# Optimization experiments

Hardware: AMD Instinct MI355X
Metric: run time of the kernel (lower is better)

## Reference

```python
import jax, jax.numpy as jnp
import numpy as np

OBS_DIM = 4096
NUM_ACTIONS = 18
ACTION_DIM = 64
D_MODEL = 512
N_LAYERS = 4
HIST = 256
BATCH = 32
D_STATE = 16
D_CONV = 4
EXPAND = 2
D_INNER = EXPAND * D_MODEL           # 1024
DT_RANK = -(-D_MODEL // 16)          # ceil(512/16)=32
OBS_OUT = D_MODEL - ACTION_DIM       # 448


def setup_inputs() -> dict:
    key = jax.random.key(0)
    ks = jax.random.split(key, 16)
    s = 0.02
    inp = {
        "obss": jax.random.normal(ks[0], (BATCH, HIST, OBS_DIM), jnp.float32),
        "actions": jax.random.randint(ks[1], (BATCH, HIST, 1), 0, NUM_ACTIONS),
        "obs_W": jax.random.normal(ks[2], (OBS_OUT, OBS_DIM), jnp.float32) * s,
        "obs_b": jnp.zeros((OBS_OUT,), jnp.float32),
        "act_emb": jax.random.normal(ks[3], (NUM_ACTIONS, ACTION_DIM), jnp.float32) * s,
        "pos_emb": jax.random.normal(ks[4], (1, HIST, D_MODEL), jnp.float32) * s,
        # stacked Mamba params, leading dim = N_LAYERS
        "W_in": jax.random.normal(ks[5], (N_LAYERS, 2 * D_INNER, D_MODEL), jnp.float32) * s,
        "conv_w": jax.random.normal(ks[6], (N_LAYERS, D_INNER, D_CONV), jnp.float32) * s,
        "conv_b": jnp.zeros((N_LAYERS, D_INNER), jnp.float32),
        "W_x": jax.random.normal(ks[7], (N_LAYERS, DT_RANK + 2 * D_STATE, D_INNER), jnp.float32) * s,
        "W_dt": jax.random.normal(ks[8], (N_LAYERS, D_INNER, DT_RANK), jnp.float32) * s,
        "b_dt": jnp.full((N_LAYERS, D_INNER), -4.6, jnp.float32),  # softplus(-4.6)~0.01
        "A_log": jnp.log(jnp.broadcast_to(jnp.arange(1, D_STATE + 1, dtype=jnp.float32), (N_LAYERS, D_INNER, D_STATE))),
        "D_p": jnp.ones((N_LAYERS, D_INNER), jnp.float32),
        "W_out": jax.random.normal(ks[9], (N_LAYERS, D_MODEL, D_INNER), jnp.float32) * s,
        "ffn_W1": jax.random.normal(ks[10], (D_MODEL, D_MODEL), jnp.float32) * s,
        "ffn_b1": jnp.zeros((D_MODEL,), jnp.float32),
        "ffn_W2": jax.random.normal(ks[11], (NUM_ACTIONS, D_MODEL), jnp.float32) * s,
        "ffn_b2": jnp.zeros((NUM_ACTIONS,), jnp.float32),
    }
    return inp


def mamba_block(x, W_in, conv_w, conv_b, W_x, W_dt, b_dt, A_log, D_p, W_out):
    # x: (B, L, D_MODEL)
    B_, L, _ = x.shape
    xz = jnp.einsum('bld,ed->ble', x, W_in)            # (B,L,2*Di)
    xi, z = jnp.split(xz, 2, axis=-1)
    # causal depthwise conv1d, kernel D_CONV
    xp = jnp.pad(xi, ((0, 0), (D_CONV - 1, 0), (0, 0)))
    xc = conv_b + sum(conv_w[:, k] * xp[:, k:k + L, :] for k in range(D_CONV))
    xc = jax.nn.silu(xc)                               # (B,L,Di)
    xdbl = jnp.einsum('bld,ed->ble', xc, W_x)          # (B,L,dt_rank+2*ds)
    dt, Bm, Cm = jnp.split(xdbl, [DT_RANK, DT_RANK + D_STATE], axis=-1)
    dt = jax.nn.softplus(jnp.einsum('blr,dr->bld', dt, W_dt) + b_dt)  # (B,L,Di)
    A = -jnp.exp(A_log)                                # (Di,ds)

    def step(h, inp):
        dt_t, B_t, C_t, x_t = inp                      # (B,Di),(B,ds),(B,ds),(B,Di)
        dA = jnp.exp(dt_t[:, :, None] * A)             # (B,Di,ds)
        h = dA * h + dt_t[:, :, None] * B_t[:, None, :] * x_t[:, :, None]
        y = jnp.einsum('bdn,bn->bd', h, C_t)
        return h, y

    h0 = jnp.zeros((B_, D_INNER, D_STATE), xc.dtype)
    xs = (dt.transpose(1, 0, 2), Bm.transpose(1, 0, 2),
          Cm.transpose(1, 0, 2), xc.transpose(1, 0, 2))
    _, ys = jax.lax.scan(step, h0, xs)                 # (L,B,Di)
    y = ys.transpose(1, 0, 2) + xc * D_p
    y = y * jax.nn.silu(z)
    return jnp.einsum('bld,ed->ble', y, W_out)         # (B,L,D_MODEL)


def reference(obss, actions, obs_W, obs_b, act_emb, pos_emb, W_in, conv_w, conv_b,
              W_x, W_dt, b_dt, A_log, D_p, W_out, ffn_W1, ffn_b1, ffn_W2, ffn_b2):
    L = obss.shape[1]
    tok = jnp.einsum('blo,eo->ble', obss, obs_W) + obs_b          # (B,L,448)
    ae = act_emb[actions[:, :, 0]]                                # (B,L,64)
    # torch.roll(ae, 1, 1) with first step zeroed (history_len > 1)
    ae = jnp.concatenate([jnp.zeros_like(ae[:, :1]), ae[:, :-1]], axis=1)
    x = jnp.concatenate([ae, tok], axis=-1) + pos_emb[:, :L, :]   # (B,L,512)
    for i in range(N_LAYERS):
        x = mamba_block(x, W_in[i], conv_w[i], conv_b[i], W_x[i], W_dt[i],
                        b_dt[i], A_log[i], D_p[i], W_out[i])
    h = jax.nn.relu(jnp.einsum('bld,ed->ble', x, ffn_W1) + ffn_b1)
    out = jnp.einsum('bld,ed->ble', h, ffn_W2) + ffn_b2           # (B,L,18)
    return out[:, -L:, :]
```

## Files before the change

kernel.cpp:

```cpp
#include <hip/hip_runtime.h>
#include <hip/hip_bf16.h>
#include <cstdint>
#include <cstddef>

#define HIST    256
#define DMODEL  512
#define DINNER  1024
#define DSTATE  16
#define DTRANK  32
#define OBSDIM  4096
#define OBSOUT  448
#define ADIM    64
#define NLAYERS 4
#define MROWS   8192

typedef __bf16  bf16x8 __attribute__((ext_vector_type(8)));
typedef float   f32x4  __attribute__((ext_vector_type(4)));

enum { MEPI_TOK = 0, MEPI_BF16 = 1, MEPI_SPLIT = 2, MEPI_RELUB = 3 };

__device__ __forceinline__ float siluf(float x) { return x / (1.f + __expf(-x)); }
__device__ __forceinline__ float softplusf(float x) {
    return fmaxf(x, 0.f) + log1pf(__expf(-fabsf(x)));
}
__device__ __forceinline__ float bflo(unsigned u) { return __uint_as_float(u << 16); }
__device__ __forceinline__ float bfhi(unsigned u) { return __uint_as_float(u & 0xffff0000u); }

template<int EPI>
__global__ __launch_bounds__(256)
void gemm_mfma(const __hip_bfloat16* __restrict__ A, int lda,
               const __hip_bfloat16* __restrict__ W,
               float* __restrict__ Cf, int ldc,
               __hip_bfloat16* __restrict__ Cb, int ldcb,
               int coff, int N, int K,
               const float* __restrict__ bias, const float* __restrict__ pos)
{
    __shared__ __hip_bfloat16 Asm[128 * 32];
    __shared__ __hip_bfloat16 Bsm[128 * 32];
    const int tid  = threadIdx.x;
    const int lane = tid & 63;
    const int wv   = tid >> 6;
    const int m0   = blockIdx.y * 128;
    const int n0   = blockIdx.x * 128;
    const int wm   = (wv >> 1) << 6;
    const int wn   = (wv & 1) << 6;
    const int sr   = lane >> 2;
    const int sc   = (lane & 3) << 3;
    const int quad = lane >> 4;
    const int c16  = lane & 15;

    f32x4 acc[4][4] = {};
    const __hip_bfloat16* aptr = A + (size_t)(m0 + wv * 16 + sr) * lda + sc;
    const __hip_bfloat16* bptr = W + (size_t)(n0 + wv * 16 + sr) * K + sc;
    __hip_bfloat16* asml = Asm + wv * 16 * 32;
    __hip_bfloat16* bsml = Bsm + wv * 16 * 32;

    for (int k0 = 0; k0 < K; k0 += 32) {
        __syncthreads();
        __builtin_amdgcn_global_load_lds(
            (const __attribute__((address_space(1))) void*)(aptr + k0),
            (__attribute__((address_space(3))) void*)(asml), 16, 0, 0);
        __builtin_amdgcn_global_load_lds(
            (const __attribute__((address_space(1))) void*)(aptr + (size_t)64 * lda + k0),
            (__attribute__((address_space(3))) void*)(asml + 64 * 32), 16, 0, 0);
        __builtin_amdgcn_global_load_lds(
            (const __attribute__((address_space(1))) void*)(bptr + k0),
            (__attribute__((address_space(3))) void*)(bsml), 16, 0, 0);
        __builtin_amdgcn_global_load_lds(
            (const __attribute__((address_space(1))) void*)(bptr + (size_t)64 * K + k0),
            (__attribute__((address_space(3))) void*)(bsml + 64 * 32), 16, 0, 0);
        __syncthreads();

        bf16x8 af[4], bfr[4];
        #pragma unroll
        for (int i = 0; i < 4; ++i) {
            af[i]  = *(const bf16x8*)(Asm + (wm + i * 16 + c16) * 32 + quad * 8);
            bfr[i] = *(const bf16x8*)(Bsm + (wn + i * 16 + c16) * 32 + quad * 8);
        }
        #pragma unroll
        for (int i = 0; i < 4; ++i)
            #pragma unroll
            for (int j = 0; j < 4; ++j)
                acc[i][j] = __builtin_amdgcn_mfma_f32_16x16x32_bf16(af[i], bfr[j], acc[i][j], 0, 0, 0);
    }

    #pragma unroll
    for (int i = 0; i < 4; ++i) {
        const int mbase = m0 + wm + i * 16 + quad * 4;
        #pragma unroll
        for (int j = 0; j < 4; ++j) {
            const int n = n0 + wn + j * 16 + c16;
            if (n < N) {
                #pragma unroll
                for (int r = 0; r < 4; ++r) {
                    const size_t m = mbase + r;
                    float v = acc[i][j][r];
                    if (EPI == MEPI_TOK) {
                        v += bias[n] + pos[(m & (HIST - 1)) * DMODEL + coff + n];
                        Cb[m * ldcb + coff + n] = __float2bfloat16(v);
                    } else if (EPI == MEPI_BF16) {
                        Cb[m * ldcb + n] = __float2bfloat16(v);
                    } else if (EPI == MEPI_SPLIT) {
                        if (n < DTRANK) Cf[m * 32 + n] = v;
                        else Cb[(m >> 1) * 64 + (n & 15) * 4 + (m & 1) * 2 + ((n >> 4) & 1)]
                                 = __float2bfloat16(v);
                    } else {
                        Cb[m * ldcb + n] = __float2bfloat16(fmaxf(v + bias[n], 0.f));
                    }
                }
            }
        }
    }
}

__global__ __launch_bounds__(256)
void gemm_f32_sp(const float* __restrict__ A, int lda,
                 const float* __restrict__ W,
                 __hip_bfloat16* __restrict__ C, int ldc,
                 int N, int K, const float* __restrict__ bias)
{
    __shared__ float As[32][68];
    __shared__ float Ws[32][68];
    const int tid = threadIdx.x;
    const int tx = tid & 15, ty = tid >> 4;
    const int m0 = blockIdx.y * 64;
    const int n0 = blockIdx.x * 64;
    const int lr = tid >> 3;
    const int lc = (tid & 7) << 2;
    float acc[4][4] = {};
    for (int k0 = 0; k0 < K; k0 += 32) {
        const float4 a0 = *(const float4*)(A + (size_t)(m0 + lr) * lda + k0 + lc);
        const float4 a1 = *(const float4*)(A + (size_t)(m0 + lr + 32) * lda + k0 + lc);
        const float4 b0 = *(const float4*)(W + (size_t)(n0 + lr) * K + k0 + lc);
        const float4 b1 = *(const float4*)(W + (size_t)(n0 + lr + 32) * K + k0 + lc);
        __syncthreads();
        As[lc+0][lr] = a0.x; As[lc+1][lr] = a0.y; As[lc+2][lr] = a0.z; As[lc+3][lr] = a0.w;
        As[lc+0][lr+32] = a1.x; As[lc+1][lr+32] = a1.y; As[lc+2][lr+32] = a1.z; As[lc+3][lr+32] = a1.w;
        Ws[lc+0][lr] = b0.x; Ws[lc+1][lr] = b0.y; Ws[lc+2][lr] = b0.z; Ws[lc+3][lr] = b0.w;
        Ws[lc+0][lr+32] = b1.x; Ws[lc+1][lr+32] = b1.y; Ws[lc+2][lr+32] = b1.z; Ws[lc+3][lr+32] = b1.w;
        __syncthreads();
        #pragma unroll
        for (int k = 0; k < 32; ++k) {
            const float4 a4 = *(const float4*)&As[k][ty << 2];
            const float4 b4 = *(const float4*)&Ws[k][tx << 2];
            const float a[4] = {a4.x, a4.y, a4.z, a4.w};
            const float b[4] = {b4.x, b4.y, b4.z, b4.w};
            #pragma unroll
            for (int i = 0; i < 4; ++i)
                #pragma unroll
                for (int j = 0; j < 4; ++j)
                    acc[i][j] = fmaf(a[i], b[j], acc[i][j]);
        }
    }
    const int mb = m0 + (ty << 2);
    const int nb = n0 + (tx << 2);
    #pragma unroll
    for (int i = 0; i < 4; ++i) {
        const size_t m = mb + i;
        #pragma unroll
        for (int j = 0; j < 4; ++j) {
            const int n = nb + j;
            C[m * ldc + n] = __float2bfloat16(softplusf(acc[i][j] + bias[n]));
        }
    }
}

__global__ __launch_bounds__(256)
void cast_bf16_kernel(const float* __restrict__ src, __hip_bfloat16* __restrict__ dst, int n4)
{
    const int i = blockIdx.x * 256 + threadIdx.x;
    if (i >= n4) return;
    const float4 v = ((const float4*)src)[i];
    union { __hip_bfloat16 h[4]; short4 s; } o;
    o.h[0] = __float2bfloat16(v.x); o.h[1] = __float2bfloat16(v.y);
    o.h[2] = __float2bfloat16(v.z); o.h[3] = __float2bfloat16(v.w);
    ((short4*)dst)[i] = o.s;
}

__global__ __launch_bounds__(256)
void cast_pad_kernel(const float* __restrict__ src, __hip_bfloat16* __restrict__ dst,
                     int nrows, int K4, int total4)
{
    const int i = blockIdx.x * 256 + threadIdx.x;
    if (i >= total4) return;
    const int row = i / K4;
    float4 v = make_float4(0.f, 0.f, 0.f, 0.f);
    if (row < nrows) v = ((const float4*)src)[i];
    union { __hip_bfloat16 h[4]; short4 s; } o;
    o.h[0] = __float2bfloat16(v.x); o.h[1] = __float2bfloat16(v.y);
    o.h[2] = __float2bfloat16(v.z); o.h[3] = __float2bfloat16(v.w);
    ((short4*)dst)[i] = o.s;
}

__global__ __launch_bounds__(256)
void embed_kernel(const int* __restrict__ actions, const float* __restrict__ act_emb,
                  const float* __restrict__ pos_emb, __hip_bfloat16* __restrict__ xb)
{
    const int idx = blockIdx.x * 256 + threadIdx.x;
    const int e = idx & 63;
    const int m = idx >> 6;
    const int l = m & (HIST - 1);
    const int b = m >> 8;
    float v = pos_emb[l * DMODEL + e];
    if (l > 0) {
        const int a = actions[b * HIST + l - 1];
        v += act_emb[a * ADIM + e];
    }
    xb[(size_t)m * DMODEL + e] = __float2bfloat16(v);
}

__global__ __launch_bounds__(256)
void conv_silu_kernel(const __hip_bfloat16* __restrict__ xzb, const float* __restrict__ cw,
                      const float* __restrict__ cb, __hip_bfloat16* __restrict__ xcb)
{
    const int idx = blockIdx.x * 256 + threadIdx.x;
    const int d = idx & (DINNER - 1);
    const int m = idx >> 10;
    const int l = m & (HIST - 1);
    const float4 w = ((const float4*)cw)[d];
    const __hip_bfloat16* basep = xzb + (size_t)m * (2 * DINNER) + d;
    float acc = cb[d] + w.w * __bfloat162float(basep[0]);
    if (l >= 1) acc = fmaf(w.z, __bfloat162float(basep[-2 * DINNER]), acc);
    if (l >= 2) acc = fmaf(w.y, __bfloat162float(basep[-4 * DINNER]), acc);
    if (l >= 3) acc = fmaf(w.x, __bfloat162float(basep[-6 * DINNER]), acc);
    xcb[idx] = __float2bfloat16(siluf(acc));
}

__device__ __forceinline__ float dpp_add(float x, const int ctrl) {
    switch (ctrl) {
    case 0xB1:  return x + __int_as_float(__builtin_amdgcn_update_dpp(0, __float_as_int(x), 0xB1, 0xF, 0xF, true));
    case 0x4E:  return x + __int_as_float(__builtin_amdgcn_update_dpp(0, __float_as_int(x), 0x4E, 0xF, 0xF, true));
    case 0x141: return x + __int_as_float(__builtin_amdgcn_update_dpp(0, __float_as_int(x), 0x141, 0xF, 0xF, true));
    default:    return x + __int_as_float(__builtin_amdgcn_update_dpp(0, __float_as_int(x), 0x140, 0xF, 0xF, true));
    }
}

__global__ __launch_bounds__(256)
void scan_kernel(const __hip_bfloat16* __restrict__ dtb, const __hip_bfloat16* __restrict__ bcb,
                 const __hip_bfloat16* __restrict__ xcb, const __hip_bfloat16* __restrict__ zb,
                 const float* __restrict__ A_log, const float* __restrict__ D_p,
                 __hip_bfloat16* __restrict__ yb)
{
    __shared__ unsigned sdx2[128][32];
    __shared__ unsigned sbc2[128][32];
    __shared__ unsigned short sz[256][16];
    const int tid = threadIdx.x;
    const int n   = tid & 15;
    const int g   = tid >> 4;
    const int c0  = blockIdx.x * 16;
    const int b   = c0 >> 10;
    const int d0  = c0 & (DINNER - 1);
    const int d   = d0 + g;
    const size_t row0 = (size_t)b * HIST;

    {
        const uint4* src = (const uint4*)((const unsigned short*)bcb + row0 * 32);
        uint4* dst = (uint4*)&sbc2[0][0];
        #pragma unroll
        for (int i = 0; i < 4; ++i) dst[tid + i * 256] = src[tid + i * 256];
    }
    {
        const int P = tid >> 1, half = tid & 1;
        const size_t m0r = row0 + 2 * P, m1r = m0r + 1;
        const unsigned short* dtu = (const unsigned short*)dtb;
        const unsigned short* xcu = (const unsigned short*)xcb;
        union { uint4 u; unsigned short s[8]; } D0, D1, X0, X1;
        D0.u = *(const uint4*)(dtu + m0r * DINNER + d0 + half * 8);
        D1.u = *(const uint4*)(dtu + m1r * DINNER + d0 + half * 8);
        X0.u = *(const uint4*)(xcu + m0r * DINNER + d0 + half * 8);
        X1.u = *(const uint4*)(xcu + m1r * DINNER + d0 + half * 8);
        #pragma unroll
        for (int gp = 0; gp < 8; ++gp) {
            sdx2[P][(half * 8 + gp) * 2]     = (unsigned)D0.s[gp] | ((unsigned)X0.s[gp] << 16);
            sdx2[P][(half * 8 + gp) * 2 + 1] = (unsigned)D1.s[gp] | ((unsigned)X1.s[gp] << 16);
        }
    }
    {
        const int l = tid >> 1, half = tid & 1;
        const unsigned short* zu = (const unsigned short*)zb;
        #pragma unroll
        for (int i = 0; i < 2; ++i) {
            const int ll = l + i * 128;
            *(uint4*)&sz[ll][half * 8] =
                *(const uint4*)(zu + (row0 + ll) * 2 * DINNER + d0 + half * 8);
        }
    }
    __syncthreads();

    const float A  = -__expf(A_log[d * DSTATE + n]);
    const float Dp = D_p[d];
    float h = 0.f;

    for (int l0 = 0; l0 < HIST; l0 += 16) {
        float yreg = 0.f;
        #pragma unroll
        for (int jp = 0; jp < 8; ++jp) {
            const int P = (l0 >> 1) + jp;
            const uint2 q  = *(const uint2*)&sdx2[P][g * 2];
            const uint2 r2 = *(const uint2*)&sbc2[P][n * 2];
            {
                const float dt = bflo(q.x), xc = bfhi(q.x);
                const float Bv = bflo(r2.x), Cv = bfhi(r2.x);
                const float dA = __expf(dt * A);
                h = fmaf(dA, h, dt * xc * Bv);
                float ctr = h * Cv;
                ctr = dpp_add(ctr, 0xB1);
                ctr = dpp_add(ctr, 0x4E);
                ctr = dpp_add(ctr, 0x141);
                ctr = dpp_add(ctr, 0x140);
                if (n == 2 * jp) yreg = ctr;
            }
            {
                const float dt = bflo(q.y), xc = bfhi(q.y);
                const float Bv = bflo(r2.y), Cv = bfhi(r2.y);
                const float dA = __expf(dt * A);
                h = fmaf(dA, h, dt * xc * Bv);
                float ctr = h * Cv;
                ctr = dpp_add(ctr, 0xB1);
                ctr = dpp_add(ctr, 0x4E);
                ctr = dpp_add(ctr, 0x141);
                ctr = dpp_add(ctr, 0x140);
                if (n == 2 * jp + 1) yreg = ctr;
            }
        }
        const int lr = l0 + n;
        const unsigned short xcu16 =
            ((const unsigned short*)sdx2)[(lr >> 1) * 64 + g * 4 + 1 + 2 * (lr & 1)];
        const float xce = bflo((unsigned)xcu16) ;
        const float xcf = __uint_as_float(((unsigned)xcu16) << 16);
        (void)xce;
        const float ze = __uint_as_float(((unsigned)sz[lr][g]) << 16);
        yb[(row0 + lr) * DINNER + d] =
            __float2bfloat16((yreg + xcf * Dp) * siluf(ze));
    }
}

__global__ __launch_bounds__(256)
void ffn2_kernel(const __hip_bfloat16* __restrict__ h, const float* __restrict__ W2,
                 const float* __restrict__ b2, float* __restrict__ out)
{
    const int idx = blockIdx.x * 256 + threadIdx.x;
    const int n = idx & 31;
    const int m = idx >> 5;
    if (n >= 18) return;
    const unsigned short* hr = (const unsigned short*)(h + (size_t)m * DMODEL);
    const float* wr = W2 + (size_t)n * DMODEL;
    float acc = b2[n];
    for (int k = 0; k < DMODEL; k += 8) {
        const uint4 hv = *(const uint4*)(hr + k);
        const float4 w0 = *(const float4*)(wr + k);
        const float4 w1 = *(const float4*)(wr + k + 4);
        acc = fmaf(bflo(hv.x), w0.x, acc);
        acc = fmaf(bfhi(hv.x), w0.y, acc);
        acc = fmaf(bflo(hv.y), w0.z, acc);
        acc = fmaf(bfhi(hv.y), w0.w, acc);
        acc = fmaf(bflo(hv.z), w1.x, acc);
        acc = fmaf(bfhi(hv.z), w1.y, acc);
        acc = fmaf(bflo(hv.w), w1.z, acc);
        acc = fmaf(bfhi(hv.w), w1.w, acc);
    }
    out[(size_t)m * 18 + n] = acc;
}

extern "C" void kernel_launch(void* const* d_in, const int* in_sizes, int n_in,
                              void* d_out, int out_size, void* d_ws, size_t ws_size,
                              hipStream_t stream)
{
    const float* obss    = (const float*)d_in[0];
    const int*   actions = (const int*)  d_in[1];
    const float* obs_W   = (const float*)d_in[2];
    const float* obs_b   = (const float*)d_in[3];
    const float* act_emb = (const float*)d_in[4];
    const float* pos_emb = (const float*)d_in[5];
    const float* W_in    = (const float*)d_in[6];
    const float* conv_w  = (const float*)d_in[7];
    const float* conv_b  = (const float*)d_in[8];
    const float* W_x     = (const float*)d_in[9];
    const float* W_dt    = (const float*)d_in[10];
    const float* b_dt    = (const float*)d_in[11];
    const float* A_log   = (const float*)d_in[12];
    const float* D_p     = (const float*)d_in[13];
    const float* W_out   = (const float*)d_in[14];
    const float* ffn_W1  = (const float*)d_in[15];
    const float* ffn_b1  = (const float*)d_in[16];
    const float* ffn_W2  = (const float*)d_in[17];
    const float* ffn_b2  = (const float*)d_in[18];
    float* out = (float*)d_out;

    const size_t MiB = 1024 * 1024;
    char* base = (char*)d_ws;
    __hip_bfloat16* xb    = (__hip_bfloat16*)(base);
    __hip_bfloat16* xzb   = (__hip_bfloat16*)(base + 8 * MiB);
    __hip_bfloat16* xcb   = (__hip_bfloat16*)(base + 40 * MiB);
    __hip_bfloat16* dtb   = (__hip_bfloat16*)(base + 56 * MiB);
    __hip_bfloat16* yb    = (__hip_bfloat16*)(base + 88 * MiB);
    float*          xdt   = (float*)(base + 104 * MiB);
    __hip_bfloat16* bcb   = (__hip_bfloat16*)(base + 105 * MiB);
    __hip_bfloat16* wbuf  = (__hip_bfloat16*)(base + 106 * MiB);
    __hip_bfloat16* wxb   = (__hip_bfloat16*)(base + 110 * MiB);
    __hip_bfloat16* obssb = (__hip_bfloat16*)(base + 8 * MiB);
    __hip_bfloat16* hbuf  = (__hip_bfloat16*)(base + 8 * MiB);

    cast_bf16_kernel<<<(MROWS * OBSDIM / 4) / 256, 256, 0, stream>>>(obss, obssb, MROWS * OBSDIM / 4);
    cast_pad_kernel<<<(512 * OBSDIM / 4) / 256, 256, 0, stream>>>(obs_W, wbuf, OBSOUT, OBSDIM / 4, 512 * OBSDIM / 4);
    embed_kernel<<<MROWS * ADIM / 256, 256, 0, stream>>>(actions, act_emb, pos_emb, xb);
    gemm_mfma<MEPI_TOK><<<dim3(4, MROWS / 128), 256, 0, stream>>>(
        obssb, OBSDIM, wbuf, nullptr, 0, xb, DMODEL, ADIM, OBSOUT, OBSDIM, obs_b, pos_emb);

    for (int i = 0; i < NLAYERS; ++i) {
        cast_bf16_kernel<<<(2 * DINNER * DMODEL / 4) / 256, 256, 0, stream>>>(
            W_in + (size_t)i * 2 * DINNER * DMODEL, wbuf, 2 * DINNER * DMODEL / 4);
        gemm_mfma<MEPI_BF16><<<dim3(2 * DINNER / 128, MROWS / 128), 256, 0, stream>>>(
            xb, DMODEL, wbuf, nullptr, 0, xzb, 2 * DINNER, 0, 2 * DINNER, DMODEL,
            nullptr, nullptr);
        conv_silu_kernel<<<MROWS * DINNER / 256, 256, 0, stream>>>(
            xzb, conv_w + (size_t)i * DINNER * 4, conv_b + (size_t)i * DINNER, xcb);
        cast_pad_kernel<<<(128 * DINNER / 4) / 256, 256, 0, stream>>>(
            W_x + (size_t)i * 64 * DINNER, wxb, 64, DINNER / 4, 128 * DINNER / 4);
        gemm_mfma<MEPI_SPLIT><<<dim3(1, MROWS / 128), 256, 0, stream>>>(
            xcb, DINNER, wxb, xdt, 0, bcb, 0, 0, 64, DINNER, nullptr, nullptr);
        gemm_f32_sp<<<dim3(DINNER / 64, MROWS / 64), 256, 0, stream>>>(
            xdt, 32, W_dt + (size_t)i * DINNER * DTRANK, dtb, DINNER, DINNER, DTRANK,
            b_dt + (size_t)i * DINNER);
        scan_kernel<<<(32 * DINNER) / 16, 256, 0, stream>>>(
            dtb, bcb, xcb, xzb + DINNER, A_log + (size_t)i * DINNER * DSTATE,
            D_p + (size_t)i * DINNER, yb);
        cast_bf16_kernel<<<(DMODEL * DINNER / 4) / 256, 256, 0, stream>>>(
            W_out + (size_t)i * DMODEL * DINNER, wbuf, DMODEL * DINNER / 4);
        gemm_mfma<MEPI_BF16><<<dim3(DMODEL / 128, MROWS / 128), 256, 0, stream>>>(
            yb, DINNER, wbuf, nullptr, 0, xb, DMODEL, 0, DMODEL, DINNER, nullptr, nullptr);
    }

    cast_bf16_kernel<<<(DMODEL * DMODEL / 4) / 256, 256, 0, stream>>>(ffn_W1, wbuf, DMODEL * DMODEL / 4);
    gemm_mfma<MEPI_RELUB><<<dim3(DMODEL / 128, MROWS / 128), 256, 0, stream>>>(
        xb, DMODEL, wbuf, nullptr, 0, hbuf, DMODEL, 0, DMODEL, DMODEL, ffn_b1, nullptr);
    ffn2_kernel<<<MROWS * 32 / 256, 256, 0, stream>>>(hbuf, ffn_W2, ffn_b2, out);
}
```

Baseline: 1.325 ms.

## Double-buffer GEMM LDS tiles and remap blocks for XCD locality

The MFMA GEMM now keeps two LDS stages and issues the next K-tile's global-to-LDS loads before computing on the current tile, with one barrier per iteration instead of two. Launches switch to a 1D grid whose block IDs are remapped so that each XCD handles a contiguous range of M tiles. The aim is to overlap memory latency with MFMA work and to improve L2 reuse per XCD. The cost is twice the LDS per block, which may reduce occupancy.

```diff
diff --git a/kernel.cpp b/kernel.cpp
--- a/kernel.cpp
+++ b/kernel.cpp
@@ -32,16 +32,22 @@
                const __hip_bfloat16* __restrict__ W,
                float* __restrict__ Cf, int ldc,
                __hip_bfloat16* __restrict__ Cb, int ldcb,
-               int coff, int N, int K,
+               int coff, int N, int K, int nbn,
                const float* __restrict__ bias, const float* __restrict__ pos)
 {
-    __shared__ __hip_bfloat16 Asm[128 * 32];
-    __shared__ __hip_bfloat16 Bsm[128 * 32];
+    __shared__ __hip_bfloat16 Asm[2][128 * 32];
+    __shared__ __hip_bfloat16 Bsm[2][128 * 32];
+    const int bid = blockIdx.x;
+    const int xcd = bid & 7;
+    const int s   = bid >> 3;
+    const int n_blk = s % nbn;
+    const int m_blk = xcd * ((int)(gridDim.x >> 3) / nbn) + s / nbn;
+    const int m0 = m_blk * 128;
+    const int n0 = n_blk * 128;
+
     const int tid  = threadIdx.x;
     const int lane = tid & 63;
     const int wv   = tid >> 6;
-    const int m0   = blockIdx.y * 128;
-    const int n0   = blockIdx.x * 128;
     const int wm   = (wv >> 1) << 6;
     const int wn   = (wv & 1) << 6;
     const int sr   = lane >> 2;
@@ -52,37 +58,46 @@
     f32x4 acc[4][4] = {};
     const __hip_bfloat16* aptr = A + (size_t)(m0 + wv * 16 + sr) * lda + sc;
     const __hip_bfloat16* bptr = W + (size_t)(n0 + wv * 16 + sr) * K + sc;
-    __hip_bfloat16* asml = Asm + wv * 16 * 32;
-    __hip_bfloat16* bsml = Bsm + wv * 16 * 32;
-
+
+#define STAGE(K0, BUF) { \
+    __hip_bfloat16* asml = Asm[BUF] + wv * 16 * 32; \
+    __hip_bfloat16* bsml = Bsm[BUF] + wv * 16 * 32; \
+    __builtin_amdgcn_global_load_lds( \
+        (const __attribute__((address_space(1))) void*)(aptr + (K0)), \
+        (__attribute__((address_space(3))) void*)(asml), 16, 0, 0); \
+    __builtin_amdgcn_global_load_lds( \
+        (const __attribute__((address_space(1))) void*)(aptr + (size_t)64 * lda + (K0)), \
+        (__attribute__((address_space(3))) void*)(asml + 64 * 32), 16, 0, 0); \
+    __builtin_amdgcn_global_load_lds( \
+        (const __attribute__((address_space(1))) void*)(bptr + (K0)), \
+        (__attribute__((address_space(3))) void*)(bsml), 16, 0, 0); \
+    __builtin_amdgcn_global_load_lds( \
+        (const __attribute__((address_space(1))) void*)(bptr + (size_t)64 * K + (K0)), \
+        (__attribute__((address_space(3))) void*)(bsml + 64 * 32), 16, 0, 0); \
+    }
+
+    STAGE(0, 0)
+    __syncthreads();
+    int cur = 0;
     for (int k0 = 0; k0 < K; k0 += 32) {
-        __syncthreads();
-        __builtin_amdgcn_global_load_lds(
-            (const __attribute__((address_space(1))) void*)(aptr + k0),
-            (__attribute__((address_space(3))) void*)(asml), 16, 0, 0);
-        __builtin_amdgcn_global_load_lds(
-            (const __attribute__((address_space(1))) void*)(aptr + (size_t)64 * lda + k0),
-            (__attribute__((address_space(3))) void*)(asml + 64 * 32), 16, 0, 0);
-        __builtin_amdgcn_global_load_lds(
-            (const __attribute__((address_space(1))) void*)(bptr + k0),
-            (__attribute__((address_space(3))) void*)(bsml), 16, 0, 0);
-        __builtin_amdgcn_global_load_lds(
-            (const __attribute__((address_space(1))) void*)(bptr + (size_t)64 * K + k0),
-            (__attribute__((address_space(3))) void*)(bsml + 64 * 32), 16, 0, 0);
-        __syncthreads();
+        if (k0 + 32 < K) STAGE(k0 + 32, cur ^ 1)
 
         bf16x8 af[4], bfr[4];
         #pragma unroll
         for (int i = 0; i < 4; ++i) {
-            af[i]  = *(const bf16x8*)(Asm + (wm + i * 16 + c16) * 32 + quad * 8);
-            bfr[i] = *(const bf16x8*)(Bsm + (wn + i * 16 + c16) * 32 + quad * 8);
+            af[i]  = *(const bf16x8*)(Asm[cur] + (wm + i * 16 + c16) * 32 + quad * 8);
+            bfr[i] = *(const bf16x8*)(Bsm[cur] + (wn + i * 16 + c16) * 32 + quad * 8);
         }
         #pragma unroll
         for (int i = 0; i < 4; ++i)
             #pragma unroll
             for (int j = 0; j < 4; ++j)
                 acc[i][j] = __builtin_amdgcn_mfma_f32_16x16x32_bf16(af[i], bfr[j], acc[i][j], 0, 0, 0);
-    }
+
+        __syncthreads();
+        cur ^= 1;
+    }
+#undef STAGE
 
     #pragma unroll
     for (int i = 0; i < 4; ++i) {
@@ -326,9 +341,7 @@
         const int lr = l0 + n;
         const unsigned short xcu16 =
             ((const unsigned short*)sdx2)[(lr >> 1) * 64 + g * 4 + 1 + 2 * (lr & 1)];
-        const float xce = bflo((unsigned)xcu16) ;
         const float xcf = __uint_as_float(((unsigned)xcu16) << 16);
-        (void)xce;
         const float ze = __uint_as_float(((unsigned)sz[lr][g]) << 16);
         yb[(row0 + lr) * DINNER + d] =
             __float2bfloat16((yreg + xcf * Dp) * siluf(ze));
@@ -404,21 +417,21 @@
     cast_bf16_kernel<<<(MROWS * OBSDIM / 4) / 256, 256, 0, stream>>>(obss, obssb, MROWS * OBSDIM / 4);
     cast_pad_kernel<<<(512 * OBSDIM / 4) / 256, 256, 0, stream>>>(obs_W, wbuf, OBSOUT, OBSDIM / 4, 512 * OBSDIM / 4);
     embed_kernel<<<MROWS * ADIM / 256, 256, 0, stream>>>(actions, act_emb, pos_emb, xb);
-    gemm_mfma<MEPI_TOK><<<dim3(4, MROWS / 128), 256, 0, stream>>>(
-        obssb, OBSDIM, wbuf, nullptr, 0, xb, DMODEL, ADIM, OBSOUT, OBSDIM, obs_b, pos_emb);
+    gemm_mfma<MEPI_TOK><<<4 * (MROWS / 128), 256, 0, stream>>>(
+        obssb, OBSDIM, wbuf, nullptr, 0, xb, DMODEL, ADIM, OBSOUT, OBSDIM, 4, obs_b, pos_emb);
 
     for (int i = 0; i < NLAYERS; ++i) {
         cast_bf16_kernel<<<(2 * DINNER * DMODEL / 4) / 256, 256, 0, stream>>>(
             W_in + (size_t)i * 2 * DINNER * DMODEL, wbuf, 2 * DINNER * DMODEL / 4);
-        gemm_mfma<MEPI_BF16><<<dim3(2 * DINNER / 128, MROWS / 128), 256, 0, stream>>>(
+        gemm_mfma<MEPI_BF16><<<(2 * DINNER / 128) * (MROWS / 128), 256, 0, stream>>>(
             xb, DMODEL, wbuf, nullptr, 0, xzb, 2 * DINNER, 0, 2 * DINNER, DMODEL,
-            nullptr, nullptr);
+            2 * DINNER / 128, nullptr, nullptr);
         conv_silu_kernel<<<MROWS * DINNER / 256, 256, 0, stream>>>(
             xzb, conv_w + (size_t)i * DINNER * 4, conv_b + (size_t)i * DINNER, xcb);
         cast_pad_kernel<<<(128 * DINNER / 4) / 256, 256, 0, stream>>>(
             W_x + (size_t)i * 64 * DINNER, wxb, 64, DINNER / 4, 128 * DINNER / 4);
-        gemm_mfma<MEPI_SPLIT><<<dim3(1, MROWS / 128), 256, 0, stream>>>(
-            xcb, DINNER, wxb, xdt, 0, bcb, 0, 0, 64, DINNER, nullptr, nullptr);
+        gemm_mfma<MEPI_SPLIT><<<MROWS / 128, 256, 0, stream>>>(
+            xcb, DINNER, wxb, xdt, 0, bcb, 0, 0, 64, DINNER, 1, nullptr, nullptr);
         gemm_f32_sp<<<dim3(DINNER / 64, MROWS / 64), 256, 0, stream>>>(
             xdt, 32, W_dt + (size_t)i * DINNER * DTRANK, dtb, DINNER, DINNER, DTRANK,
             b_dt + (size_t)i * DINNER);
@@ -427,12 +440,14 @@
             D_p + (size_t)i * DINNER, yb);
         cast_bf16_kernel<<<(DMODEL * DINNER / 4) / 256, 256, 0, stream>>>(
             W_out + (size_t)i * DMODEL * DINNER, wbuf, DMODEL * DINNER / 4);
-        gemm_mfma<MEPI_BF16><<<dim3(DMODEL / 128, MROWS / 128), 256, 0, stream>>>(
-            yb, DINNER, wbuf, nullptr, 0, xb, DMODEL, 0, DMODEL, DINNER, nullptr, nullptr);
+        gemm_mfma<MEPI_BF16><<<(DMODEL / 128) * (MROWS / 128), 256, 0, stream>>>(
+            yb, DINNER, wbuf, nullptr, 0, xb, DMODEL, 0, DMODEL, DINNER,
+            DMODEL / 128, nullptr, nullptr);
     }
 
     cast_bf16_kernel<<<(DMODEL * DMODEL / 4) / 256, 256, 0, stream>>>(ffn_W1, wbuf, DMODEL * DMODEL / 4);
-    gemm_mfma<MEPI_RELUB><<<dim3(DMODEL / 128, MROWS / 128), 256, 0, stream>>>(
-        xb, DMODEL, wbuf, nullptr, 0, hbuf, DMODEL, 0, DMODEL, DMODEL, ffn_b1, nullptr);
+    gemm_mfma<MEPI_RELUB><<<(DMODEL / 128) * (MROWS / 128), 256, 0, stream>>>(
+        xb, DMODEL, wbuf, nullptr, 0, hbuf, DMODEL, 0, DMODEL, DMODEL,
+        DMODEL / 128, ffn_b1, nullptr);
     ffn2_kernel<<<MROWS * 32 / 256, 256, 0, stream>>>(hbuf, ffn_W2, ffn_b2, out);
 }
```

Result: faster. 1.282 ms (-3.2%).
